# Performance work log

Measured on AMD Instinct MI355X. Metric: run time of the kernel, lower is better.

Reference implementation:

```python
import jax, jax.numpy as jnp
import numpy as np

DN = ('NCHW', 'OIHW', 'NCHW')
HEADS = 4
EPS_LN = 1e-5
EPS_NORM = 1e-12


def conv(x, w, pad=0, groups=1):
    return jax.lax.conv_general_dilated(
        x, w, window_strides=(1, 1), padding=[(pad, pad), (pad, pad)],
        dimension_numbers=DN, feature_group_count=groups)


def layernorm(x, w, b):
    # LayerNorm over channel axis per spatial position (to_3d -> LN(c) -> to_4d)
    mu = jnp.mean(x, axis=1, keepdims=True)
    var = jnp.mean((x - mu) ** 2, axis=1, keepdims=True)
    return (x - mu) / jnp.sqrt(var + EPS_LN) * w[None, :, None, None] + b[None, :, None, None]


def setup_inputs() -> dict:
    key = jax.random.key(0)
    ks = jax.random.split(key, 12)
    b, dim, h, w = 2, 192, 128, 128
    hidden = int(dim * 2.66)  # 510

    def rn(k, shape, scale=0.05):
        return jax.random.normal(k, shape, dtype=jnp.float32) * scale

    return {
        'x': jax.random.normal(ks[0], (b, dim, h, w), dtype=jnp.float32),
        'illum': jax.random.normal(ks[1], (b, dim, h, w), dtype=jnp.float32),
        'ln1_w': jnp.ones((dim,), jnp.float32), 'ln1_b': jnp.zeros((dim,), jnp.float32),
        'lnL_w': jnp.ones((dim,), jnp.float32), 'lnL_b': jnp.zeros((dim,), jnp.float32),
        'ln2_w': jnp.ones((dim,), jnp.float32), 'ln2_b': jnp.zeros((dim,), jnp.float32),
        'q_w': rn(ks[2], (dim, dim, 1, 1)),
        'qdw_w': rn(ks[3], (dim, dim, 3, 3)),        # full 3x3 conv (no groups in source)
        'kv_w': rn(ks[4], (2 * dim, dim, 1, 1)),
        'kvdw_w': rn(ks[5], (2 * dim, 1, 3, 3)),     # depthwise, groups = 2*dim
        'temp': jnp.ones((HEADS, 1, 1), jnp.float32),
        'proj_w': rn(ks[6], (dim, dim, 1, 1)),
        'pin_w': rn(ks[7], (hidden, dim, 1, 1)),
        'dw_w': rn(ks[8], (hidden, hidden, 3, 3)),   # full 3x3 conv (no groups in source)
        'pout_w': rn(ks[9], (dim, hidden, 1, 1)),
    }


def _block(x, illum, ln1_w, ln1_b, lnL_w, lnL_b, ln2_w, ln2_b,
           q_w, qdw_w, kv_w, kvdw_w, temp, proj_w, pin_w, dw_w, pout_w):
    b, c, h, w = x.shape
    ch = c // HEADS

    # ---- Illum-guided channel attention (MDTA) ----
    xn = layernorm(x, ln1_w, ln1_b)
    iln = layernorm(illum, lnL_w, lnL_b)
    q = conv(conv(iln, q_w), qdw_w, pad=1)
    kv = conv(conv(xn, kv_w), kvdw_w, pad=1, groups=2 * c)
    k, v = jnp.split(kv, 2, axis=1)

    def split_heads(t):
        return t.reshape(b, HEADS, ch, h * w)  # b head c (hw)

    q, k, v = split_heads(q), split_heads(k), split_heads(v)
    q = q / jnp.maximum(jnp.linalg.norm(q, axis=-1, keepdims=True), EPS_NORM)
    k = k / jnp.maximum(jnp.linalg.norm(k, axis=-1, keepdims=True), EPS_NORM)

    attn = jnp.einsum('bhce,bhde->bhcd', q, k) * temp[None]  # [b, head, ch, ch]
    attn = jax.nn.softmax(attn, axis=-1)
    out = jnp.einsum('bhcd,bhde->bhce', attn, v).reshape(b, c, h, w)
    x = x + conv(out, proj_w)

    # ---- FFN: 1x1 -> full 3x3 -> GELU -> 1x1 ----
    xn2 = layernorm(x, ln2_w, ln2_b)
    f = conv(xn2, pin_w)
    f = jax.nn.gelu(conv(f, dw_w, pad=1), approximate=False)
    x = x + conv(f, pout_w)
    return x


def reference(x, illum, ln1_w, ln1_b, lnL_w, lnL_b, ln2_w, ln2_b,
              q_w, qdw_w, kv_w, kvdw_w, temp, proj_w, pin_w, dw_w, pout_w):
    return _block(x, illum, ln1_w, ln1_b, lnL_w, lnL_b, ln2_w, ln2_b,
                  q_w, qdw_w, kv_w, kvdw_w, temp, proj_w, pin_w, dw_w, pout_w)
```

## Files before the change

kernel.cpp:

```cpp
#include <hip/hip_runtime.h>
#include <hip/hip_bf16.h>

typedef __hip_bfloat16 bf16;
typedef __attribute__((ext_vector_type(8))) short bf16x8v;
typedef __attribute__((ext_vector_type(4))) float f32x4;

namespace {
constexpr int B_  = 2;
constexpr int C_  = 192;
constexpr int HW_ = 128 * 128;
constexpr int C2_ = 384;
}

static __device__ __forceinline__ float fb(bf16 v) { return __bfloat162float(v); }
static __device__ __forceinline__ bf16 tob(float v) { return __float2bfloat16(v); }

typedef __attribute__((address_space(1))) const char GChar;
typedef __attribute__((address_space(3))) char LChar;
static __device__ __forceinline__ void gl16(const void* g, void* l) {
    __builtin_amdgcn_global_load_lds((GChar*)g, (LChar*)l, 16, 0, 0);
}
static __device__ __forceinline__ bf16x8v lread(const bf16* base, int row, int slot) {
    const char* p = (const char*)base + (size_t)row * 128 + ((size_t)((slot ^ (row & 7))) << 4);
    return *(const bf16x8v*)p;
}

static __device__ __forceinline__ void rp1(const float* W, bf16* Wr, int blk, int t,
                                           int N, int K, int Npad, int Kpad) {
    int i = blk * 256 + t;
    if (i >= Npad * Kpad) return;
    int n = i / Kpad, k = i % Kpad;
    float v = (n < N && k < K) ? W[n * K + k] : 0.f;
    Wr[i] = tob(v);
}
static __device__ __forceinline__ void rp3(const float* W, bf16* Wr, int blk, int t,
                                           int N, int K, int Npad, int Kpad) {
    int i = blk * 256 + t;
    int NK = Npad * Kpad;
    if (i >= NK) return;
    int n = i / Kpad, k = i % Kpad;
    if (n < N && k < K) {
        const float* src = W + ((size_t)(n * K + k)) * 9;
#pragma unroll
        for (int q = 0; q < 9; q++) Wr[(size_t)q * NK + i] = tob(src[q]);
    } else {
#pragma unroll
        for (int q = 0; q < 9; q++) Wr[(size_t)q * NK + i] = tob(0.f);
    }
}
__global__ __launch_bounds__(256) void k_repack_all(
    const float* __restrict__ qw, const float* __restrict__ kvw,
    const float* __restrict__ projw, const float* __restrict__ pinw,
    const float* __restrict__ poutw, const float* __restrict__ qdww,
    const float* __restrict__ dww,
    bf16* __restrict__ Wq1, bf16* __restrict__ Wkv, bf16* __restrict__ Wproj,
    bf16* __restrict__ Wpin, bf16* __restrict__ Wpout, bf16* __restrict__ Wqdw,
    bf16* __restrict__ Wdw, char* __restrict__ zpage) {
    int blk = blockIdx.x, t = threadIdx.x;
    if (blk < 144)        rp1(qw,    Wq1,   blk,        t, 192, 192, 192, 192);
    else if (blk < 432)   rp1(kvw,   Wkv,   blk - 144,  t, 384, 192, 384, 192);
    else if (blk < 576)   rp1(projw, Wproj, blk - 432,  t, 192, 192, 192, 192);
    else if (blk < 960)   rp1(pinw,  Wpin,  blk - 576,  t, 510, 192, 512, 192);
    else if (blk < 1344)  rp1(poutw, Wpout, blk - 960,  t, 192, 510, 192, 512);
    else if (blk < 1488)  rp3(qdww,  Wqdw,  blk - 1344, t, 192, 192, 192, 192);
    else if (blk < 2512)  rp3(dww,   Wdw,   blk - 1488, t, 510, 510, 512, 512);
    else ((uint4*)zpage)[t] = make_uint4(0u, 0u, 0u, 0u);
}

__global__ __launch_bounds__(256) void k_ln_nchw(const float* __restrict__ X0,
                                                 const float* __restrict__ X1,
                                                 const float* __restrict__ w0,
                                                 const float* __restrict__ b0,
                                                 const float* __restrict__ w1,
                                                 const float* __restrict__ b1,
                                                 bf16* __restrict__ out0,
                                                 bf16* __restrict__ out1) {
    const float* X = blockIdx.y ? X1 : X0;
    const float* w = blockIdx.y ? w1 : w0;
    const float* bb = blockIdx.y ? b1 : b0;
    bf16* out = blockIdx.y ? out1 : out0;
    __shared__ float lds[64][C_ + 1];
    int t = threadIdx.x;
    int p0 = blockIdx.x * 64;
    int b = p0 / HW_, pi0 = p0 % HW_;
    for (int i = t; i < 64 * C_ / 4; i += 256) {
        int c = i >> 4, pp4 = (i & 15) << 2;
        float4 v = *(const float4*)(X + ((size_t)(b * C_ + c)) * HW_ + pi0 + pp4);
        lds[pp4 + 0][c] = v.x; lds[pp4 + 1][c] = v.y;
        lds[pp4 + 2][c] = v.z; lds[pp4 + 3][c] = v.w;
    }
    __syncthreads();
    int pp = t >> 2, qq = t & 3;
    float s = 0.f, s2 = 0.f;
    for (int c = qq * 48; c < qq * 48 + 48; c++) { float v = lds[pp][c]; s += v; s2 += v * v; }
    s  += __shfl_xor(s, 1);  s  += __shfl_xor(s, 2);
    s2 += __shfl_xor(s2, 1); s2 += __shfl_xor(s2, 2);
    float mu = s / C_;
    float rstd = rsqrtf(s2 / C_ - mu * mu + 1e-5f);
    bf16* ob = out + ((size_t)(p0 + pp)) * C_ + qq * 48;
#pragma unroll
    for (int j = 0; j < 6; j++) {
        union { bf16 h[8]; uint4 u; } ov;
#pragma unroll
        for (int e = 0; e < 8; e++) {
            int c = qq * 48 + j * 8 + e;
            ov.h[e] = tob((lds[pp][c] - mu) * rstd * w[c] + bb[c]);
        }
        *(uint4*)(ob + j * 8) = ov.u;
    }
}

__global__ __launch_bounds__(256) void k_ln_pc(const bf16* __restrict__ X2,
                                               const float* __restrict__ w,
                                               const float* __restrict__ bb,
                                               bf16* __restrict__ out) {
    int t = threadIdx.x;
    int p = blockIdx.x * 64 + (t >> 2), qq = t & 3;
    const bf16* row = X2 + (size_t)p * C_ + qq * 48;
    uint4 u[6];
#pragma unroll
    for (int j = 0; j < 6; j++) u[j] = *(const uint4*)(row + j * 8);
    float s = 0.f, s2 = 0.f;
#pragma unroll
    for (int j = 0; j < 6; j++) {
        const bf16* pv = (const bf16*)&u[j];
#pragma unroll
        for (int e = 0; e < 8; e++) { float v = fb(pv[e]); s += v; s2 += v * v; }
    }
    s  += __shfl_xor(s, 1);  s  += __shfl_xor(s, 2);
    s2 += __shfl_xor(s2, 1); s2 += __shfl_xor(s2, 2);
    float mu = s / C_;
    float rstd = rsqrtf(s2 / C_ - mu * mu + 1e-5f);
    bf16* orow = out + (size_t)p * C_ + qq * 48;
#pragma unroll
    for (int j = 0; j < 6; j++) {
        const bf16* pv = (const bf16*)&u[j];
        union { bf16 h[8]; uint4 u4; } ov;
#pragma unroll
        for (int e = 0; e < 8; e++) {
            int c = qq * 48 + j * 8 + e;
            ov.h[e] = tob((fb(pv[e]) - mu) * rstd * w[c] + bb[c]);
        }
        *(uint4*)(orow + j * 8) = ov.u4;
    }
}

template <int BN, int EPI>
__global__ __launch_bounds__(256) void k_gemm1x1(const bf16* __restrict__ A,
                                                 const bf16* __restrict__ Wr,
                                                 const int K, const int Cout,
                                                 void* __restrict__ outp,
                                                 const void* __restrict__ resid,
                                                 const int wbstride) {
    constexpr int WN = BN / 2, FN = WN / 16, BIT = BN / 32;
    __shared__ __align__(16) bf16 As[128 * 64];
    __shared__ __align__(16) bf16 Bs[BN * 64];
    const int t = threadIdx.x;
    const int mt = blockIdx.x;
    const int n0 = blockIdx.y * BN;
    const int b = mt >> 7, y = mt & 127;
    const int w = t >> 6, lane = t & 63;
    const int wm = w >> 1, wn = w & 1;
    const int g = lane >> 4, r = lane & 15;
    const int ldw = t - lane;

    f32x4 acc[4][FN];
#pragma unroll
    for (int i = 0; i < 4; i++)
#pragma unroll
        for (int j = 0; j < FN; j++) acc[i][j] = {0.f, 0.f, 0.f, 0.f};

    const bf16* Abase = A + (size_t)mt * 128 * K;
    const bf16* Wbase = Wr + (size_t)b * wbstride;

    for (int c0 = 0; c0 < K; c0 += 64) {
#pragma unroll
        for (int it = 0; it < 4; it++) {
            int idx = it * 256 + t;
            int row = idx >> 3, sl = idx & 7;
            const char* gp = (const char*)(Abase + (size_t)row * K + c0) + ((sl ^ (row & 7)) << 4);
            gl16(gp, (char*)As + (size_t)(it * 256 + ldw) * 16);
        }
#pragma unroll
        for (int it = 0; it < BIT; it++) {
            int idx = it * 256 + t;
            int row = idx >> 3, sl = idx & 7;
            const char* gp = (const char*)(Wbase + (size_t)(n0 + row) * K + c0) + ((sl ^ (row & 7)) << 4);
            gl16(gp, (char*)Bs + (size_t)(it * 256 + ldw) * 16);
        }
        __syncthreads();
#pragma unroll
        for (int ks = 0; ks < 2; ks++) {
            bf16x8v af[4], bv[FN];
#pragma unroll
            for (int fm = 0; fm < 4; fm++)
                af[fm] = lread(As, wm * 64 + fm * 16 + r, ks * 4 + g);
#pragma unroll
            for (int fn = 0; fn < FN; fn++)
                bv[fn] = lread(Bs, wn * WN + fn * 16 + r, ks * 4 + g);
#pragma unroll
            for (int fm = 0; fm < 4; fm++)
#pragma unroll
                for (int fn = 0; fn < FN; fn++)
                    acc[fm][fn] = __builtin_amdgcn_mfma_f32_16x16x32_bf16(af[fm], bv[fn], acc[fm][fn], 0, 0, 0);
        }
        __syncthreads();
    }

#pragma unroll
    for (int fm = 0; fm < 4; fm++)
#pragma unroll
        for (int fn = 0; fn < FN; fn++)
#pragma unroll
            for (int reg = 0; reg < 4; reg++) {
                int xl = wm * 64 + fm * 16 + g * 4 + reg;
                int co = n0 + wn * WN + fn * 16 + r;
                float v = acc[fm][fn][reg];
                if constexpr (EPI == 1) {
                    ((bf16*)outp)[((size_t)mt * 128 + xl) * Cout + co] = tob(v);
                } else if constexpr (EPI == 2) {
                    v += ((const float*)resid)[((size_t)(b * C_ + co)) * HW_ + y * 128 + xl];
                    ((bf16*)outp)[((size_t)mt * 128 + xl) * C_ + co] = tob(v);
                } else {
                    v += fb(((const bf16*)resid)[((size_t)mt * 128 + xl) * C_ + co]);
                    ((float*)outp)[((size_t)(b * C_ + co)) * HW_ + y * 128 + xl] = v;
                }
            }
}

template <int BN, int EPI>
__global__ __launch_bounds__(256) void k_gemm3x3(const bf16* __restrict__ A,
                                                 const bf16* __restrict__ Wr,
                                                 const int Cin, const int Cout,
                                                 bf16* __restrict__ outp,
                                                 const char* __restrict__ zpage) {
    constexpr int WN = BN / 2, FN = WN / 16, BIT = BN / 32;
    __shared__ __align__(16) bf16 As[160 * 64];
    __shared__ __align__(16) bf16 Bs[BN * 64];
    const int t = threadIdx.x;
    const int mtRaw = blockIdx.x;
    const int mt = ((mtRaw & 7) << 5) | (mtRaw >> 3);
    const int n0 = blockIdx.y * BN;
    const int b = mt >> 7, y = mt & 127;
    const int w = t >> 6, lane = t & 63;
    const int wm = w >> 1, wn = w & 1;
    const int g = lane >> 4, r = lane & 15;
    const int ldw = t - lane;

    f32x4 acc[4][FN];
#pragma unroll
    for (int i = 0; i < 4; i++)
#pragma unroll
        for (int j = 0; j < FN; j++) acc[i][j] = {0.f, 0.f, 0.f, 0.f};

    for (int ky = 0; ky < 3; ky++) {
        const int yy = y + ky - 1;
        if (yy < 0 || yy > 127) continue;
        const bf16* Ab = A + ((size_t)b * HW_ + (size_t)yy * 128) * Cin;
        for (int c0 = 0; c0 < Cin; c0 += 64) {
            for (int kx = 0; kx < 3; kx++) {
                if (kx == 0) {
#pragma unroll
                    for (int it = 0; it < 5; it++) {
                        int idx = it * 256 + t;
                        int row = idx >> 3, sl = idx & 7;
                        int so = (sl ^ (row & 7)) << 4;
                        const char* gp = (row >= 1 && row <= 128)
                            ? (const char*)(Ab + (size_t)(row - 1) * Cin + c0) + so
                            : zpage + so;
                        gl16(gp, (char*)As + (size_t)(it * 256 + ldw) * 16);
                    }
                }
                const bf16* Wb = Wr + (size_t)(ky * 3 + kx) * Cout * Cin;
#pragma unroll
                for (int it = 0; it < BIT; it++) {
                    int idx = it * 256 + t;
                    int row = idx >> 3, sl = idx & 7;
                    const char* gp = (const char*)(Wb + (size_t)(n0 + row) * Cin + c0) + ((sl ^ (row & 7)) << 4);
                    gl16(gp, (char*)Bs + (size_t)(it * 256 + ldw) * 16);
                }
                __syncthreads();
#pragma unroll
                for (int ks = 0; ks < 2; ks++) {
                    bf16x8v af[4], bv[FN];
#pragma unroll
                    for (int fm = 0; fm < 4; fm++)
                        af[fm] = lread(As, wm * 64 + fm * 16 + r + kx, ks * 4 + g);
#pragma unroll
                    for (int fn = 0; fn < FN; fn++)
                        bv[fn] = lread(Bs, wn * WN + fn * 16 + r, ks * 4 + g);
#pragma unroll
                    for (int fm = 0; fm < 4; fm++)
#pragma unroll
                        for (int fn = 0; fn < FN; fn++)
                            acc[fm][fn] = __builtin_amdgcn_mfma_f32_16x16x32_bf16(af[fm], bv[fn], acc[fm][fn], 0, 0, 0);
                }
                __syncthreads();
            }
        }
    }
#pragma unroll
    for (int fm = 0; fm < 4; fm++)
#pragma unroll
        for (int fn = 0; fn < FN; fn++)
#pragma unroll
            for (int reg = 0; reg < 4; reg++) {
                int xl = wm * 64 + fm * 16 + g * 4 + reg;
                int co = n0 + wn * WN + fn * 16 + r;
                float v = acc[fm][fn][reg];
                if constexpr (EPI == 1) v = 0.5f * v * (1.0f + erff(v * 0.70710678118654752f));
                outp[((size_t)mt * 128 + xl) * Cout + co] = tob(v);
            }
}

__global__ __launch_bounds__(192) void k_dwconv2(const bf16* __restrict__ kv,
                                                 const float* __restrict__ wdw,
                                                 bf16* __restrict__ kout,
                                                 bf16* __restrict__ vout) {
    __shared__ float wlds[1728];
    const int t = threadIdx.x;
    const int row = blockIdx.x;
    const int z = blockIdx.y;
    const int b = row >> 7, y = row & 127;
    for (int i = t; i < 432; i += 192)
        ((float4*)wlds)[i] = ((const float4*)(wdw + (size_t)z * 1728))[i];
    __syncthreads();
    const int c8h = t % 24, xg = t / 24;
    const int cbase = z * C_ + c8h * 8;
    float wreg[9][8];
#pragma unroll
    for (int tap = 0; tap < 9; tap++)
#pragma unroll
        for (int j = 0; j < 8; j++) wreg[tap][j] = wlds[(c8h * 8 + j) * 9 + tap];

    bf16* outb = (z == 0 ? kout : vout) + (size_t)(b * HW_ + y * 128) * C_ + c8h * 8;
    const uint4 zero4 = make_uint4(0u, 0u, 0u, 0u);
    const int x0 = xg * 16;
    bool vy[3]; const bf16* rowp[3];
#pragma unroll
    for (int ky = 0; ky < 3; ky++) {
        int yy = y + ky - 1;
        vy[ky] = (yy >= 0 && yy <= 127);
        int yyc = vy[ky] ? yy : 0;
        rowp[ky] = kv + ((size_t)b * HW_ + (size_t)yyc * 128) * C2_ + cbase;
    }
    uint4 win[3][3];
#pragma unroll
    for (int ky = 0; ky < 3; ky++) {
        win[ky][0] = (vy[ky] && x0 - 1 >= 0) ? *(const uint4*)(rowp[ky] + (size_t)(x0 - 1) * C2_) : zero4;
        win[ky][1] = vy[ky] ? *(const uint4*)(rowp[ky] + (size_t)x0 * C2_) : zero4;
    }
    for (int i = 0; i < 16; i++) {
        int x = x0 + i;
#pragma unroll
        for (int ky = 0; ky < 3; ky++)
            win[ky][2] = (vy[ky] && x + 1 <= 127) ? *(const uint4*)(rowp[ky] + (size_t)(x + 1) * C2_) : zero4;
        float acc[8];
#pragma unroll
        for (int j = 0; j < 8; j++) acc[j] = 0.f;
#pragma unroll
        for (int ky = 0; ky < 3; ky++)
#pragma unroll
            for (int kx = 0; kx < 3; kx++) {
                const bf16* pv = (const bf16*)&win[ky][kx];
#pragma unroll
                for (int j = 0; j < 8; j++)
                    acc[j] += fb(pv[j]) * wreg[ky * 3 + kx][j];
            }
        union { bf16 h[8]; uint4 u; } ov;
#pragma unroll
        for (int j = 0; j < 8; j++) ov.h[j] = tob(acc[j]);
        *(uint4*)(outb + (size_t)x * C_) = ov.u;
#pragma unroll
        for (int ky = 0; ky < 3; ky++) { win[ky][0] = win[ky][1]; win[ky][1] = win[ky][2]; }
    }
}

__global__ __launch_bounds__(256) void k_qk(const bf16* __restrict__ q,
                                            const bf16* __restrict__ k,
                                            float* __restrict__ Spart,
                                            float* __restrict__ ssq) {
    __shared__ float qs[64][49];
    __shared__ float ks[64][49];
    __shared__ float redq[4][48], redk[4][48];
    int t = threadIdx.x;
    int ch = blockIdx.x, hd = blockIdx.y, b = blockIdx.z;
    int i0 = (t >> 4) * 3, j0 = (t & 15) * 3;
    int cs = t % 48, qr = t / 48;
    float acc[3][3];
    float sq = 0.f, sk = 0.f;
#pragma unroll
    for (int a = 0; a < 3; a++)
#pragma unroll
        for (int c = 0; c < 3; c++) acc[a][c] = 0.f;

    for (int sub = 0; sub < 4; sub++) {
        size_t rbase = ((size_t)b * HW_ + ch * 256 + sub * 64) * C_ + hd * 48;
        for (int i = t; i < 64 * 6; i += 256) {
            int row = i / 6, oc = i % 6;
            uint4 v = *(const uint4*)(q + rbase + (size_t)row * C_ + oc * 8);
            const bf16* pv = (const bf16*)&v;
#pragma unroll
            for (int j = 0; j < 8; j++) qs[row][oc * 8 + j] = fb(pv[j]);
            uint4 v2 = *(const uint4*)(k + rbase + (size_t)row * C_ + oc * 8);
            const bf16* pv2 = (const bf16*)&v2;
#pragma unroll
            for (int j = 0; j < 8; j++) ks[row][oc * 8 + j] = fb(pv2[j]);
        }
        __syncthreads();
        if (t < 192) {
#pragma unroll
            for (int rr = 0; rr < 16; rr++) {
                float qv = qs[qr * 16 + rr][cs]; sq += qv * qv;
                float kv2 = ks[qr * 16 + rr][cs]; sk += kv2 * kv2;
            }
        }
        for (int p = 0; p < 64; p++) {
            float a0 = qs[p][i0], a1 = qs[p][i0 + 1], a2 = qs[p][i0 + 2];
            float b0 = ks[p][j0], b1 = ks[p][j0 + 1], b2 = ks[p][j0 + 2];
            acc[0][0] += a0 * b0; acc[0][1] += a0 * b1; acc[0][2] += a0 * b2;
            acc[1][0] += a1 * b0; acc[1][1] += a1 * b1; acc[1][2] += a1 * b2;
            acc[2][0] += a2 * b0; acc[2][1] += a2 * b1; acc[2][2] += a2 * b2;
        }
        __syncthreads();
    }
    if (t < 192) { redq[qr][cs] = sq; redk[qr][cs] = sk; }
    float* dst = Spart + (((size_t)(b * 4 + hd)) * 64 + ch) * 2304;
#pragma unroll
    for (int a = 0; a < 3; a++)
#pragma unroll
        for (int c = 0; c < 3; c++) dst[(i0 + a) * 48 + (j0 + c)] = acc[a][c];
    __syncthreads();
    if (t < 48) {
        float s0 = redq[0][t] + redq[1][t] + redq[2][t] + redq[3][t];
        float s1 = redk[0][t] + redk[1][t] + redk[2][t] + redk[3][t];
        ssq[((size_t)b * 64 + ch) * C_ + hd * 48 + t] = s0;
        ssq[((size_t)(2 + b) * 64 + ch) * C_ + hd * 48 + t] = s1;
    }
}

__global__ __launch_bounds__(256) void k_softmax(const float* __restrict__ Spart,
                                                 const float* __restrict__ ssq,
                                                 const float* __restrict__ temp,
                                                 bf16* __restrict__ attnW) {
    __shared__ float S[2304];
    __shared__ float invk_s[48];
    int t = threadIdx.x;
    int hd = blockIdx.x, b = blockIdx.y;
    const float* base = Spart + ((size_t)(b * 4 + hd)) * 64 * 2304;
    for (int e = t; e < 2304; e += 256) {
        float s = 0.f;
        for (int ch = 0; ch < 64; ch++) s += base[(size_t)ch * 2304 + e];
        S[e] = s;
    }
    if (t < 48) {
        int c = hd * 48 + t;
        float sk = 0.f;
        for (int ch = 0; ch < 64; ch++) sk += ssq[((size_t)(2 + b) * 64 + ch) * C_ + c];
        invk_s[t] = 1.f / fmaxf(sqrtf(sk), 1e-12f);
    }
    __syncthreads();
    if (t >= 48) return;
    int c = hd * 48 + t;
    float sq = 0.f;
    for (int ch = 0; ch < 64; ch++) sq += ssq[((size_t)b * 64 + ch) * C_ + c];
    float qi = 1.f / fmaxf(sqrtf(sq), 1e-12f);
    float tp = temp[hd];
    float row[48];
    float mx = -1e30f;
    for (int j = 0; j < 48; j++) {
        float s = S[t * 48 + j] * qi * invk_s[j] * tp;
        row[j] = s;
        mx = fmaxf(mx, s);
    }
    float sum = 0.f;
    for (int j = 0; j < 48; j++) { row[j] = expf(row[j] - mx); sum += row[j]; }
    float is = 1.f / sum;
    bf16* wrow = attnW + ((size_t)b * 192 + hd * 48 + t) * 192;
    for (int blk4 = 0; blk4 < 4; blk4++)
        for (int j = 0; j < 48; j++)
            wrow[blk4 * 48 + j] = tob(blk4 == hd ? row[j] * is : 0.f);
}

extern "C" void kernel_launch(void* const* d_in, const int* in_sizes, int n_in,
                              void* d_out, int out_size, void* d_ws, size_t ws_size,
                              hipStream_t stream) {
    const float* x     = (const float*)d_in[0];
    const float* illum = (const float*)d_in[1];
    const float* ln1w  = (const float*)d_in[2];
    const float* ln1b  = (const float*)d_in[3];
    const float* lnLw  = (const float*)d_in[4];
    const float* lnLb  = (const float*)d_in[5];
    const float* ln2w  = (const float*)d_in[6];
    const float* ln2b  = (const float*)d_in[7];
    const float* qw    = (const float*)d_in[8];
    const float* qdww  = (const float*)d_in[9];
    const float* kvw   = (const float*)d_in[10];
    const float* kvdww = (const float*)d_in[11];
    const float* temp  = (const float*)d_in[12];
    const float* projw = (const float*)d_in[13];
    const float* pinw  = (const float*)d_in[14];
    const float* dww   = (const float*)d_in[15];
    const float* poutw = (const float*)d_in[16];

    char* ws = (char*)d_ws;
    bf16*  Wq1   = (bf16*)(ws + 0);
    bf16*  Wkv   = (bf16*)(ws + 73728);
    bf16*  Wqdw  = (bf16*)(ws + 221184);
    bf16*  Wproj = (bf16*)(ws + 884736);
    bf16*  Wpin  = (bf16*)(ws + 958464);
    bf16*  Wdw   = (bf16*)(ws + 1155072);
    bf16*  Wpout = (bf16*)(ws + 5873664);
    float* ssq   = (float*)(ws + 6070272);
    char*  zpage = (char*)(ws + 6266880);
    const size_t A0 = 6270976, u = 12582912;
    bf16* xn    = (bf16*)(ws + A0 + 0 * u);
    bf16* iln   = (bf16*)(ws + A0 + 1 * u);
    bf16* qtmp  = (bf16*)(ws + A0 + 2 * u);
    bf16* qb    = (bf16*)(ws + A0 + 1 * u);
    bf16* kvtmp = (bf16*)(ws + A0 + 2 * u);
    bf16* kb    = (bf16*)(ws + A0 + 0 * u);
    bf16* vb    = (bf16*)(ws + A0 + 4 * u);
    float* Spart = (float*)(ws + A0 + 3 * u);
    bf16*  attnW = (bf16*)(ws + A0 + 3 * u + 4718592);
    bf16* outa  = (bf16*)(ws + A0 + 2 * u);
    bf16* x2    = (bf16*)(ws + A0 + 0 * u);
    bf16* xn2   = (bf16*)(ws + A0 + 3 * u);
    bf16* fbuf  = (bf16*)(ws + A0 + 4 * u);
    bf16* gbuf  = (bf16*)(ws + A0 + 1 * u);

    k_repack_all<<<2513, 256, 0, stream>>>(qw, kvw, projw, pinw, poutw, qdww, dww,
                                           Wq1, Wkv, Wproj, Wpin, Wpout, Wqdw, Wdw, zpage);

    k_ln_nchw<<<dim3(512, 2), 256, 0, stream>>>(x, illum, ln1w, ln1b, lnLw, lnLb, xn, iln);

    k_gemm1x1<96, 1><<<dim3(256, 2), 256, 0, stream>>>(iln, Wq1, 192, 192, qtmp, nullptr, 0);
    k_gemm3x3<96, 0><<<dim3(256, 2), 256, 0, stream>>>(qtmp, Wqdw, 192, 192, qb, zpage);

    k_gemm1x1<128, 1><<<dim3(256, 3), 256, 0, stream>>>(xn, Wkv, 192, 384, kvtmp, nullptr, 0);
    k_dwconv2<<<dim3(256, 2), 192, 0, stream>>>(kvtmp, kvdww, kb, vb);

    k_qk<<<dim3(64, 4, 2), 256, 0, stream>>>(qb, kb, Spart, ssq);
    k_softmax<<<dim3(4, 2), 256, 0, stream>>>(Spart, ssq, temp, attnW);
    k_gemm1x1<96, 1><<<dim3(256, 2), 256, 0, stream>>>(vb, attnW, 192, 192, outa, nullptr, 36864);

    k_gemm1x1<96, 2><<<dim3(256, 2), 256, 0, stream>>>(outa, Wproj, 192, 192, x2, x, 0);

    k_ln_pc<<<512, 256, 0, stream>>>(x2, ln2w, ln2b, xn2);
    k_gemm1x1<128, 1><<<dim3(256, 4), 256, 0, stream>>>(xn2, Wpin, 192, 512, fbuf, nullptr, 0);
    k_gemm3x3<128, 1><<<dim3(256, 4), 256, 0, stream>>>(fbuf, Wdw, 512, 512, gbuf, zpage);
    k_gemm1x1<96, 3><<<dim3(256, 2), 256, 0, stream>>>(gbuf, Wpout, 512, 192, d_out, x2, 0);
}
```

Baseline: 380.8 us.

## Fold projection into attention weights and merge repack/LN and q/kv GEMM launches

Precomputes Mw = proj_w · blockdiag(attn) per batch with a small kernel, so the attention-apply and output projection become a single 1x1 GEMM with residual. The weight repack kernel is merged with the two input LayerNorms, and the q and kv 1x1 GEMMs are launched together in one grid. This removes one full activation GEMM pass and several launches, at the cost of a larger workspace footprint for the relocated buffers.

```diff
diff --git a/kernel.cpp b/kernel.cpp
--- a/kernel.cpp
+++ b/kernel.cpp
@@ -48,40 +48,36 @@
         for (int q = 0; q < 9; q++) Wr[(size_t)q * NK + i] = tob(0.f);
     }
 }
-__global__ __launch_bounds__(256) void k_repack_all(
+
+__global__ __launch_bounds__(256) void k_repack_ln(
     const float* __restrict__ qw, const float* __restrict__ kvw,
     const float* __restrict__ projw, const float* __restrict__ pinw,
     const float* __restrict__ poutw, const float* __restrict__ qdww,
     const float* __restrict__ dww,
     bf16* __restrict__ Wq1, bf16* __restrict__ Wkv, bf16* __restrict__ Wproj,
     bf16* __restrict__ Wpin, bf16* __restrict__ Wpout, bf16* __restrict__ Wqdw,
-    bf16* __restrict__ Wdw, char* __restrict__ zpage) {
+    bf16* __restrict__ Wdw, char* __restrict__ zpage,
+    const float* __restrict__ X0, const float* __restrict__ X1,
+    const float* __restrict__ w0, const float* __restrict__ b0,
+    const float* __restrict__ w1, const float* __restrict__ b1,
+    bf16* __restrict__ out0, bf16* __restrict__ out1) {
+    __shared__ float lds[64][C_ + 1];
     int blk = blockIdx.x, t = threadIdx.x;
-    if (blk < 144)        rp1(qw,    Wq1,   blk,        t, 192, 192, 192, 192);
-    else if (blk < 432)   rp1(kvw,   Wkv,   blk - 144,  t, 384, 192, 384, 192);
-    else if (blk < 576)   rp1(projw, Wproj, blk - 432,  t, 192, 192, 192, 192);
-    else if (blk < 960)   rp1(pinw,  Wpin,  blk - 576,  t, 510, 192, 512, 192);
-    else if (blk < 1344)  rp1(poutw, Wpout, blk - 960,  t, 192, 510, 192, 512);
-    else if (blk < 1488)  rp3(qdww,  Wqdw,  blk - 1344, t, 192, 192, 192, 192);
-    else if (blk < 2512)  rp3(dww,   Wdw,   blk - 1488, t, 510, 510, 512, 512);
-    else ((uint4*)zpage)[t] = make_uint4(0u, 0u, 0u, 0u);
-}
-
-__global__ __launch_bounds__(256) void k_ln_nchw(const float* __restrict__ X0,
-                                                 const float* __restrict__ X1,
-                                                 const float* __restrict__ w0,
-                                                 const float* __restrict__ b0,
-                                                 const float* __restrict__ w1,
-                                                 const float* __restrict__ b1,
-                                                 bf16* __restrict__ out0,
-                                                 bf16* __restrict__ out1) {
-    const float* X = blockIdx.y ? X1 : X0;
-    const float* w = blockIdx.y ? w1 : w0;
-    const float* bb = blockIdx.y ? b1 : b0;
-    bf16* out = blockIdx.y ? out1 : out0;
-    __shared__ float lds[64][C_ + 1];
-    int t = threadIdx.x;
-    int p0 = blockIdx.x * 64;
+    if (blk < 144)        { rp1(qw,    Wq1,   blk,        t, 192, 192, 192, 192); return; }
+    else if (blk < 432)   { rp1(kvw,   Wkv,   blk - 144,  t, 384, 192, 384, 192); return; }
+    else if (blk < 576)   { rp1(projw, Wproj, blk - 432,  t, 192, 192, 192, 192); return; }
+    else if (blk < 960)   { rp1(pinw,  Wpin,  blk - 576,  t, 510, 192, 512, 192); return; }
+    else if (blk < 1344)  { rp1(poutw, Wpout, blk - 960,  t, 192, 510, 192, 512); return; }
+    else if (blk < 1488)  { rp3(qdww,  Wqdw,  blk - 1344, t, 192, 192, 192, 192); return; }
+    else if (blk < 2512)  { rp3(dww,   Wdw,   blk - 1488, t, 510, 510, 512, 512); return; }
+    else if (blk == 2512) { ((uint4*)zpage)[t] = make_uint4(0u, 0u, 0u, 0u); return; }
+    int lb = blk - 2513;
+    int sel = lb >> 9, xb = lb & 511;
+    const float* X = sel ? X1 : X0;
+    const float* w = sel ? w1 : w0;
+    const float* bb = sel ? b1 : b0;
+    bf16* out = sel ? out1 : out0;
+    int p0 = xb * 64;
     int b = p0 / HW_, pi0 = p0 % HW_;
     for (int i = t; i < 64 * C_ / 4; i += 256) {
         int c = i >> 4, pp4 = (i & 15) << 2;
@@ -146,18 +142,16 @@
 }
 
 template <int BN, int EPI>
-__global__ __launch_bounds__(256) void k_gemm1x1(const bf16* __restrict__ A,
-                                                 const bf16* __restrict__ Wr,
-                                                 const int K, const int Cout,
-                                                 void* __restrict__ outp,
-                                                 const void* __restrict__ resid,
-                                                 const int wbstride) {
+static __device__ __forceinline__ void gemm1x1_body(const bf16* __restrict__ A,
+                                                    const bf16* __restrict__ Wbase,
+                                                    const int K, const int Cout,
+                                                    void* __restrict__ outp,
+                                                    const void* __restrict__ resid,
+                                                    const int mt, const int n0) {
     constexpr int WN = BN / 2, FN = WN / 16, BIT = BN / 32;
     __shared__ __align__(16) bf16 As[128 * 64];
     __shared__ __align__(16) bf16 Bs[BN * 64];
     const int t = threadIdx.x;
-    const int mt = blockIdx.x;
-    const int n0 = blockIdx.y * BN;
     const int b = mt >> 7, y = mt & 127;
     const int w = t >> 6, lane = t & 63;
     const int wm = w >> 1, wn = w & 1;
@@ -171,7 +165,6 @@
         for (int j = 0; j < FN; j++) acc[i][j] = {0.f, 0.f, 0.f, 0.f};
 
     const bf16* Abase = A + (size_t)mt * 128 * K;
-    const bf16* Wbase = Wr + (size_t)b * wbstride;
 
     for (int c0 = 0; c0 < K; c0 += 64) {
 #pragma unroll
@@ -226,6 +219,33 @@
                     ((float*)outp)[((size_t)(b * C_ + co)) * HW_ + y * 128 + xl] = v;
                 }
             }
+}
+
+template <int BN, int EPI>
+__global__ __launch_bounds__(256) void k_gemm1x1(const bf16* __restrict__ A,
+                                                 const bf16* __restrict__ Wr,
+                                                 const int K, const int Cout,
+                                                 void* __restrict__ outp,
+                                                 const void* __restrict__ resid,
+                                                 const int wbstride) {
+    const int mt = blockIdx.x;
+    const bf16* Wbase = Wr + (size_t)(mt >> 7) * wbstride;
+    gemm1x1_body<BN, EPI>(A, Wbase, K, Cout, outp, resid, mt, blockIdx.y * BN);
+}
+
+__global__ __launch_bounds__(256) void k_qkv(const bf16* __restrict__ iln,
+                                             const bf16* __restrict__ xn,
+                                             const bf16* __restrict__ Wq1,
+                                             const bf16* __restrict__ Wkv,
+                                             bf16* __restrict__ qtmp,
+                                             bf16* __restrict__ kvtmp) {
+    const bool isq = blockIdx.y < 2;
+    const bf16* A = isq ? iln : xn;
+    const bf16* Wr = isq ? Wq1 : Wkv;
+    bf16* outp = isq ? qtmp : kvtmp;
+    const int Cout = isq ? 192 : 384;
+    const int n0 = (isq ? blockIdx.y : blockIdx.y - 2) * 96;
+    gemm1x1_body<96, 1>(A, Wr, 192, Cout, outp, nullptr, blockIdx.x, n0);
 }
 
 template <int BN, int EPI>
@@ -476,10 +496,32 @@
     float sum = 0.f;
     for (int j = 0; j < 48; j++) { row[j] = expf(row[j] - mx); sum += row[j]; }
     float is = 1.f / sum;
-    bf16* wrow = attnW + ((size_t)b * 192 + hd * 48 + t) * 192;
-    for (int blk4 = 0; blk4 < 4; blk4++)
-        for (int j = 0; j < 48; j++)
-            wrow[blk4 * 48 + j] = tob(blk4 == hd ? row[j] * is : 0.f);
+    bf16* wrow = attnW + ((size_t)b * 192 + hd * 48 + t) * 192 + hd * 48;
+    for (int j = 0; j < 48; j++) wrow[j] = tob(row[j] * is);
+}
+
+__global__ __launch_bounds__(256) void k_wav(const bf16* __restrict__ Wproj,
+                                             const bf16* __restrict__ attnW,
+                                             bf16* __restrict__ Mw) {
+    int bid = blockIdx.x;
+    int b = bid / 12, rg = bid % 12;
+    int t = threadIdx.x;
+    int row = rg * 16 + (t >> 4);
+    int c0b = (t & 15) * 12;
+    int hd = c0b / 48;
+    const bf16* aw = attnW + (size_t)b * 36864;
+    float acc[12];
+#pragma unroll
+    for (int j = 0; j < 12; j++) acc[j] = 0.f;
+    for (int k = hd * 48; k < hd * 48 + 48; k++) {
+        float wp = fb(Wproj[row * 192 + k]);
+        const bf16* ar = aw + (size_t)k * 192 + c0b;
+#pragma unroll
+        for (int j = 0; j < 12; j++) acc[j] += wp * fb(ar[j]);
+    }
+    bf16* mrow = Mw + ((size_t)b * 192 + row) * 192 + c0b;
+#pragma unroll
+    for (int j = 0; j < 12; j++) mrow[j] = tob(acc[j]);
 }
 
 extern "C" void kernel_launch(void* const* d_in, const int* in_sizes, int n_in,
@@ -519,32 +561,34 @@
     bf16* qtmp  = (bf16*)(ws + A0 + 2 * u);
     bf16* qb    = (bf16*)(ws + A0 + 1 * u);
     bf16* kvtmp = (bf16*)(ws + A0 + 2 * u);
-    bf16* kb    = (bf16*)(ws + A0 + 0 * u);
     bf16* vb    = (bf16*)(ws + A0 + 4 * u);
     float* Spart = (float*)(ws + A0 + 3 * u);
     bf16*  attnW = (bf16*)(ws + A0 + 3 * u + 4718592);
-    bf16* outa  = (bf16*)(ws + A0 + 2 * u);
+    bf16*  Mw    = (bf16*)(ws + A0 + 3 * u + 4866048);
+    bf16* kb    = (bf16*)(ws + A0 + 0 * u);
     bf16* x2    = (bf16*)(ws + A0 + 0 * u);
     bf16* xn2   = (bf16*)(ws + A0 + 3 * u);
     bf16* fbuf  = (bf16*)(ws + A0 + 4 * u);
     bf16* gbuf  = (bf16*)(ws + A0 + 1 * u);
-
-    k_repack_all<<<2513, 256, 0, stream>>>(qw, kvw, projw, pinw, poutw, qdww, dww,
-                                           Wq1, Wkv, Wproj, Wpin, Wpout, Wqdw, Wdw, zpage);
-
-    k_ln_nchw<<<dim3(512, 2), 256, 0, stream>>>(x, illum, ln1w, ln1b, lnLw, lnLb, xn, iln);
-
-    k_gemm1x1<96, 1><<<dim3(256, 2), 256, 0, stream>>>(iln, Wq1, 192, 192, qtmp, nullptr, 0);
+    qtmp  = (bf16*)(ws + A0 + 4 * u);
+    kvtmp = (bf16*)(ws + A0 + 2 * u);
+    qb    = (bf16*)(ws + A0 + 1 * u);
+    vb    = (bf16*)(ws + A0 + 4 * u + 12582912);
+
+    k_repack_ln<<<3537, 256, 0, stream>>>(qw, kvw, projw, pinw, poutw, qdww, dww,
+                                          Wq1, Wkv, Wproj, Wpin, Wpout, Wqdw, Wdw, zpage,
+                                          x, illum, ln1w, ln1b, lnLw, lnLb, xn, iln);
+
+    k_qkv<<<dim3(256, 6), 256, 0, stream>>>(iln, xn, Wq1, Wkv, qtmp, kvtmp);
+
     k_gemm3x3<96, 0><<<dim3(256, 2), 256, 0, stream>>>(qtmp, Wqdw, 192, 192, qb, zpage);
-
-    k_gemm1x1<128, 1><<<dim3(256, 3), 256, 0, stream>>>(xn, Wkv, 192, 384, kvtmp, nullptr, 0);
     k_dwconv2<<<dim3(256, 2), 192, 0, stream>>>(kvtmp, kvdww, kb, vb);
 
     k_qk<<<dim3(64, 4, 2), 256, 0, stream>>>(qb, kb, Spart, ssq);
     k_softmax<<<dim3(4, 2), 256, 0, stream>>>(Spart, ssq, temp, attnW);
-    k_gemm1x1<96, 1><<<dim3(256, 2), 256, 0, stream>>>(vb, attnW, 192, 192, outa, nullptr, 36864);
-
-    k_gemm1x1<96, 2><<<dim3(256, 2), 256, 0, stream>>>(outa, Wproj, 192, 192, x2, x, 0);
+    k_wav<<<24, 256, 0, stream>>>(Wproj, attnW, Mw);
+
+    k_gemm1x1<96, 2><<<dim3(256, 2), 256, 0, stream>>>(vb, Mw, 192, 192, x2, x, 36864);
 
     k_ln_pc<<<512, 256, 0, stream>>>(x2, ln2w, ln2b, xn2);
     k_gemm1x1<128, 1><<<dim3(256, 4), 256, 0, stream>>>(xn2, Wpin, 192, 512, fbuf, nullptr, 0);
```

Measured after the change: 371.8 us. 2.4% less time.
